# Kernel optimization log

Hardware: AMD Instinct MI355X
Metric: run time of the kernel (lower is better)

The kernel has to match this reference:

```python
import jax, jax.numpy as jnp
import numpy as np

H, D_MODEL, LEN_Q, LEN_K, D_K, D_V = 16, 1024, 512, 2048, 64, 64
B = 4

def setup_inputs() -> dict:
    key = jax.random.key(0)
    ks = jax.random.split(key, 16)
    s = 0.02
    return {
        "Q": jax.random.normal(ks[0], (B, LEN_Q, D_MODEL), jnp.float32),
        "K": jax.random.normal(ks[1], (B, LEN_K, D_MODEL), jnp.float32),
        "V": jax.random.normal(ks[2], (B, LEN_K, D_MODEL), jnp.float32),
        "node_num": LEN_Q,
        "mask": jax.random.randint(ks[3], (B, LEN_K), 0, 2, jnp.int32),
        # params (stored as [in, out] so y = x @ W + b)
        "Wq": jax.random.normal(ks[4], (D_MODEL, H * D_K), jnp.float32) * s,
        "bq": jnp.zeros((H * D_K,), jnp.float32),
        "Wk": jax.random.normal(ks[5], (D_MODEL, H * D_K), jnp.float32) * s,
        "bk": jnp.zeros((H * D_K,), jnp.float32),
        "Wv": jax.random.normal(ks[6], (D_MODEL, H * D_V), jnp.float32) * s,
        "bv": jnp.zeros((H * D_V,), jnp.float32),
        "Wo": jax.random.normal(ks[7], (H * D_V, D_MODEL), jnp.float32) * s,
        "bo": jnp.zeros((D_MODEL,), jnp.float32),
        "gamma": jnp.ones((D_MODEL,), jnp.float32),
        "beta": jnp.zeros((D_MODEL,), jnp.float32),
    }

def _layernorm(x, gamma, beta, eps=1e-5):
    mu = jnp.mean(x, axis=-1, keepdims=True)
    var = jnp.mean((x - mu) ** 2, axis=-1, keepdims=True)
    return (x - mu) * jax.lax.rsqrt(var + eps) * gamma + beta

def reference(Q, K, V, node_num, mask, Wq, bq, Wk, bk, Wv, bv, Wo, bo, gamma, beta):
    b, lq, _ = Q.shape
    lk = K.shape[1]
    q = (Q @ Wq + bq).reshape(b, lq, H, D_K)   # [B, Lq, h, dk]
    k = (K @ Wk + bk).reshape(b, lk, H, D_K)   # [B, Lk, h, dk]
    v = (V @ Wv + bv).reshape(b, lk, H, D_V)   # [B, Lk, h, dv]
    scores = jnp.einsum('bqhd,bkhd->bhqk', q, k) / jnp.sqrt(jnp.float32(D_K))
    scores = jnp.where(mask[:, None, None, :] == 0, -jnp.inf, scores)
    alpha = jax.nn.softmax(scores, axis=-1)    # [B, h, Lq, Lk]
    out = jnp.einsum('bhqk,bkhd->bqhd', alpha, v).reshape(b, lq, H * D_V)
    out = out @ Wo + bo + Q                    # dropout is identity (eval)
    return _layernorm(out, gamma, beta)
```

## Files before the change

### kernel.cpp

```cpp
#include <hip/hip_runtime.h>

typedef __attribute__((ext_vector_type(8))) __bf16 bf16x8;
typedef __attribute__((ext_vector_type(4))) float f32x4;
typedef __attribute__((ext_vector_type(8))) unsigned short u16x8;

__device__ __forceinline__ float bf2f(unsigned short h) {
  union { unsigned int u; float f; } a; a.u = ((unsigned int)h) << 16; return a.f;
}
__device__ __forceinline__ unsigned short f2bf(float f) {
  union { float f; unsigned int u; } a; a.f = f;
  unsigned int u = a.u;
  u += 0x7fffu + ((u >> 16) & 1u);
  return (unsigned short)(u >> 16);
}
__device__ __forceinline__ float fast_exp2(float x) {
#if __has_builtin(__builtin_amdgcn_exp2f)
  return __builtin_amdgcn_exp2f(x);
#else
  return exp2f(x);
#endif
}
__device__ __forceinline__ bf16x8 ld_frag(const unsigned short* p) {
  bf16x8 r; __builtin_memcpy(&r, p, 16); return r;
}
__device__ __forceinline__ void cp16(unsigned short* dst, const unsigned short* src) {
  u16x8 t; __builtin_memcpy(&t, src, 16); __builtin_memcpy(dst, &t, 16);
}

#if __has_builtin(__builtin_amdgcn_global_load_lds)
typedef __attribute__((address_space(3))) unsigned int lds_u32;
typedef const __attribute__((address_space(1))) unsigned int glb_u32;
__device__ __forceinline__ void gload16(const unsigned short* g, unsigned short* l) {
  __builtin_amdgcn_global_load_lds((glb_u32*)g, (lds_u32*)l, 16, 0, 0);
}
#else
__device__ __forceinline__ void gload16(const unsigned short* g, unsigned short* l) {
  cp16(l, g);
}
#endif

__global__ __launch_bounds__(256) void cvt_kernel(
    const float* __restrict__ in, unsigned short* __restrict__ out, int n8)
{
  int i = blockIdx.x * 256 + threadIdx.x;
  if (i >= n8) return;
  float tf[8]; __builtin_memcpy(tf, &in[(size_t)i * 8], 32);
  unsigned short tu[8];
#pragma unroll
  for (int j = 0; j < 8; j++) tu[j] = f2bf(tf[j]);
  __builtin_memcpy(&out[(size_t)i * 8], tu, 16);
}

__global__ __launch_bounds__(256) void transpose4_kernel(
    const float* __restrict__ w0, const float* __restrict__ w1,
    const float* __restrict__ w2, const float* __restrict__ w3,
    unsigned short* __restrict__ out)
{
  __shared__ unsigned short tile[64 * 65];
  const int z = blockIdx.z;
  const float* in = (z == 0) ? w0 : (z == 1) ? w1 : (z == 2) ? w2 : w3;
  unsigned short* o = out + (size_t)z * 1048576;
  const int dim = 1024;
  const int t = threadIdx.x;
  const int n0 = blockIdx.x * 64, k0 = blockIdx.y * 64;
#pragma unroll
  for (int e = 0; e < 16; e++) {
    int idx = e * 256 + t;
    int i = idx >> 6, j = idx & 63;
    tile[i * 65 + j] = f2bf(in[(size_t)(k0 + i) * dim + n0 + j]);
  }
  __syncthreads();
#pragma unroll
  for (int e = 0; e < 16; e++) {
    int idx = e * 256 + t;
    int i = idx >> 6, j = idx & 63;
    o[(size_t)(n0 + i) * dim + k0 + j] = tile[j * 65 + i];
  }
}

__global__ __launch_bounds__(256) void gemm_kt_kernel(
    const unsigned short* __restrict__ A,
    const unsigned short* __restrict__ BT,
    const float* __restrict__ bias,
    unsigned short* __restrict__ C,
    int M, int N, int K)
{
  __shared__ unsigned short As[2][128 * 32];
  __shared__ unsigned short Bs[2][128 * 32];
  const int tid  = threadIdx.x;
  const int wave = tid >> 6;
  const int lane = tid & 63;
  const int quad = lane >> 4;
  const int l16  = lane & 15;
  const int m0 = blockIdx.x * 128;
  const int n0 = blockIdx.y * 128;
  const int wm = (wave & 1) * 64;
  const int wn = (wave >> 1) * 64;

  const f32x4 fz = {0.0f, 0.0f, 0.0f, 0.0f};
  f32x4 acc[4][4];
#pragma unroll
  for (int i = 0; i < 4; i++)
#pragma unroll
    for (int j = 0; j < 4; j++) acc[i][j] = fz;

  const int srow0 = tid >> 2;
  const int srow1 = srow0 + 64;
  const int scol  = (tid & 3) * 8;

  auto stage = [&](int bf, int k0) {
    gload16(&A[(size_t)(m0 + srow0) * K + k0 + scol], &As[bf][srow0 * 32 + scol]);
    gload16(&A[(size_t)(m0 + srow1) * K + k0 + scol], &As[bf][srow1 * 32 + scol]);
    gload16(&BT[(size_t)(n0 + srow0) * K + k0 + scol], &Bs[bf][srow0 * 32 + scol]);
    gload16(&BT[(size_t)(n0 + srow1) * K + k0 + scol], &Bs[bf][srow1 * 32 + scol]);
  };

  const int NT = K >> 5;
  stage(0, 0);
  for (int kt = 0; kt < NT; ++kt) {
    const int cur = kt & 1;
    if (kt + 1 < NT) {
      stage(cur ^ 1, (kt + 1) << 5);
      asm volatile("s_waitcnt vmcnt(4)" ::: "memory");
    } else {
      asm volatile("s_waitcnt vmcnt(0)" ::: "memory");
    }
    __builtin_amdgcn_s_barrier();
    bf16x8 afr[4], bfr[4];
#pragma unroll
    for (int mt = 0; mt < 4; mt++) afr[mt] = ld_frag(&As[cur][(wm + mt * 16 + l16) * 32 + quad * 8]);
#pragma unroll
    for (int nt = 0; nt < 4; nt++) bfr[nt] = ld_frag(&Bs[cur][(wn + nt * 16 + l16) * 32 + quad * 8]);
#pragma unroll
    for (int mt = 0; mt < 4; mt++)
#pragma unroll
      for (int nt = 0; nt < 4; nt++)
        acc[mt][nt] = __builtin_amdgcn_mfma_f32_16x16x32_bf16(afr[mt], bfr[nt], acc[mt][nt], 0, 0, 0);
    __builtin_amdgcn_s_barrier();
  }

#pragma unroll
  for (int nt = 0; nt < 4; nt++) {
    const int col = n0 + wn + nt * 16 + l16;
    const float bvv = bias[col];
    const int h  = col >> 6;
    const int dk = col & 63;
    const int dkoff = (dk >> 5) * 512 + ((dk >> 3) & 3) * 8 + (dk & 7);
#pragma unroll
    for (int mt = 0; mt < 4; mt++) {
#pragma unroll
      for (int r = 0; r < 4; r++) {
        const int row = m0 + wm + mt * 16 + quad * 4 + r;
        const int bb = row >> 11, key = row & 2047;
        const size_t tile = ((size_t)((bb * 16 + h) * 32 + (key >> 6))) * 4096;
        C[tile + ((key & 63) >> 4) * 1024 + (key & 15) * 32 + dkoff] =
            f2bf(acc[mt][nt][r] + bvv);
      }
    }
  }
}

__global__ __launch_bounds__(256) void gemm_bt64_kernel(
    const unsigned short* __restrict__ A,
    const unsigned short* __restrict__ BT,
    const float* __restrict__ bias,
    unsigned short* __restrict__ C,
    int M, int N, int K, float cscale)
{
  __shared__ unsigned short As[2][64 * 32];
  __shared__ unsigned short Bs[2][128 * 32];
  const int tid  = threadIdx.x;
  const int wave = tid >> 6;
  const int lane = tid & 63;
  const int quad = lane >> 4;
  const int l16  = lane & 15;
  const int m0 = blockIdx.x * 64;
  const int n0 = blockIdx.y * 128;
  const int wm = (wave & 1) * 32;
  const int wn = (wave >> 1) * 64;

  const f32x4 fz = {0.0f, 0.0f, 0.0f, 0.0f};
  f32x4 acc[2][4];
#pragma unroll
  for (int i = 0; i < 2; i++)
#pragma unroll
    for (int j = 0; j < 4; j++) acc[i][j] = fz;

  const int srow0 = tid >> 2;
  const int srow1 = srow0 + 64;
  const int scol  = (tid & 3) * 8;

  auto stage = [&](int bf, int k0) {
    gload16(&A[(size_t)(m0 + srow0) * K + k0 + scol], &As[bf][srow0 * 32 + scol]);
    gload16(&BT[(size_t)(n0 + srow0) * K + k0 + scol], &Bs[bf][srow0 * 32 + scol]);
    gload16(&BT[(size_t)(n0 + srow1) * K + k0 + scol], &Bs[bf][srow1 * 32 + scol]);
  };

  const int NT = K >> 5;
  stage(0, 0);
  for (int kt = 0; kt < NT; ++kt) {
    const int cur = kt & 1;
    if (kt + 1 < NT) {
      stage(cur ^ 1, (kt + 1) << 5);
      asm volatile("s_waitcnt vmcnt(3)" ::: "memory");
    } else {
      asm volatile("s_waitcnt vmcnt(0)" ::: "memory");
    }
    __builtin_amdgcn_s_barrier();
    bf16x8 afr[2], bfr[4];
#pragma unroll
    for (int mt = 0; mt < 2; mt++) afr[mt] = ld_frag(&As[cur][(wm + mt * 16 + l16) * 32 + quad * 8]);
#pragma unroll
    for (int nt = 0; nt < 4; nt++) bfr[nt] = ld_frag(&Bs[cur][(wn + nt * 16 + l16) * 32 + quad * 8]);
#pragma unroll
    for (int mt = 0; mt < 2; mt++)
#pragma unroll
      for (int nt = 0; nt < 4; nt++)
        acc[mt][nt] = __builtin_amdgcn_mfma_f32_16x16x32_bf16(afr[mt], bfr[nt], acc[mt][nt], 0, 0, 0);
    __builtin_amdgcn_s_barrier();
  }

#pragma unroll
  for (int nt = 0; nt < 4; nt++) {
    int col = n0 + wn + nt * 16 + l16;
    float bv = bias[col];
#pragma unroll
    for (int mt = 0; mt < 2; mt++) {
      int rowb = m0 + wm + mt * 16 + quad * 4;
#pragma unroll
      for (int r = 0; r < 4; r++)
        C[(size_t)(rowb + r) * N + col] = f2bf((acc[mt][nt][r] + bv) * cscale);
    }
  }
}

__global__ __launch_bounds__(256) void gemm_vt_kernel(
    const unsigned short* __restrict__ A,
    const unsigned short* __restrict__ BT,
    const float* __restrict__ bias,
    unsigned short* __restrict__ vt)
{
  __shared__ unsigned short As[2][128 * 32];
  __shared__ unsigned short Bs[2][128 * 32];
  __shared__ unsigned short Ts[4][64 * 72];
  const int K = 1024;
  const int tid  = threadIdx.x;
  const int wave = tid >> 6;
  const int lane = tid & 63;
  const int quad = lane >> 4;
  const int l16  = lane & 15;
  const int m0 = blockIdx.x * 128;
  const int n0 = blockIdx.y * 128;
  const int wm = (wave & 1) * 64;
  const int wn = (wave >> 1) * 64;

  const f32x4 fz = {0.0f, 0.0f, 0.0f, 0.0f};
  f32x4 acc[4][4];
#pragma unroll
  for (int i = 0; i < 4; i++)
#pragma unroll
    for (int j = 0; j < 4; j++) acc[i][j] = fz;

  const int srow0 = tid >> 2;
  const int srow1 = srow0 + 64;
  const int scol  = (tid & 3) * 8;

  auto stage = [&](int bf, int k0) {
    gload16(&A[(size_t)(m0 + srow0) * K + k0 + scol], &As[bf][srow0 * 32 + scol]);
    gload16(&A[(size_t)(m0 + srow1) * K + k0 + scol], &As[bf][srow1 * 32 + scol]);
    gload16(&BT[(size_t)(n0 + srow0) * K + k0 + scol], &Bs[bf][srow0 * 32 + scol]);
    gload16(&BT[(size_t)(n0 + srow1) * K + k0 + scol], &Bs[bf][srow1 * 32 + scol]);
  };

  const int NT = K >> 5;
  stage(0, 0);
  for (int kt = 0; kt < NT; ++kt) {
    const int cur = kt & 1;
    if (kt + 1 < NT) {
      stage(cur ^ 1, (kt + 1) << 5);
      asm volatile("s_waitcnt vmcnt(4)" ::: "memory");
    } else {
      asm volatile("s_waitcnt vmcnt(0)" ::: "memory");
    }
    __builtin_amdgcn_s_barrier();
    bf16x8 afr[4], bfr[4];
#pragma unroll
    for (int mt = 0; mt < 4; mt++) afr[mt] = ld_frag(&As[cur][(wm + mt * 16 + l16) * 32 + quad * 8]);
#pragma unroll
    for (int nt = 0; nt < 4; nt++) bfr[nt] = ld_frag(&Bs[cur][(wn + nt * 16 + l16) * 32 + quad * 8]);
#pragma unroll
    for (int mt = 0; mt < 4; mt++)
#pragma unroll
      for (int nt = 0; nt < 4; nt++)
        acc[mt][nt] = __builtin_amdgcn_mfma_f32_16x16x32_bf16(afr[mt], bfr[nt], acc[mt][nt], 0, 0, 0);
    __builtin_amdgcn_s_barrier();
  }

#pragma unroll
  for (int nt = 0; nt < 4; nt++) {
    float bv = bias[n0 + wn + nt * 16 + l16];
#pragma unroll
    for (int mt = 0; mt < 4; mt++)
#pragma unroll
      for (int r = 0; r < 4; r++)
        Ts[wave][(nt * 16 + l16) * 72 + mt * 16 + quad * 4 + r] = f2bf(acc[mt][nt][r] + bv);
  }
  {
    const int R0 = m0 + wm;
    const int b  = R0 >> 11;
    const int key0 = R0 & 2047;
    const int h   = (n0 + wn) >> 6;
    const int dv  = lane;
    const int ktile = key0 >> 6;
    const size_t vtile = ((size_t)((b * 16 + h) * 32 + ktile)) * 4096;
    const size_t dbase = vtile + (size_t)(dv >> 4) * 1024 + (dv & 15) * 32;
#pragma unroll
    for (int jb = 0; jb < 8; jb++)
      cp16((unsigned short*)&vt[dbase + (jb >> 2) * 512 + (jb & 3) * 8],
           &Ts[wave][lane * 72 + jb * 8]);
  }
}

__global__ __launch_bounds__(256) void attn_kernel(
    const unsigned short* __restrict__ qp,
    const unsigned short* __restrict__ kp,
    const unsigned short* __restrict__ vt,
    const int* __restrict__ mask,
    unsigned short* __restrict__ attn)
{
  __shared__ unsigned short Kb[2][4096];
  __shared__ unsigned short Vb[2][4096];
  __shared__ int Ms[2048];
  __shared__ unsigned short Ps[4][16 * 72];

  const int tid  = threadIdx.x;
  const int wave = tid >> 6;
  const int lane = tid & 63;
  const int quad = lane >> 4;
  const int l16  = lane & 15;
  const int bid  = blockIdx.x;
  const int bh = bid & 63;
  const int qg = bid >> 6;
  const int b = bh >> 4, h = bh & 15;

  bf16x8 aq[2];
  {
    const size_t qbase = ((size_t)(b * 512 + qg * 64 + wave * 16 + l16)) * 1024 + h * 64;
#pragma unroll
    for (int kc = 0; kc < 2; kc++)
      aq[kc] = ld_frag(&qp[qbase + kc * 32 + quad * 8]);
  }
  {
    const unsigned short* mg = (const unsigned short*)(mask + b * 2048);
    unsigned short* ml = (unsigned short*)Ms;
    gload16(mg + tid * 8, ml + tid * 8);
    gload16(mg + 2048 + tid * 8, ml + 2048 + tid * 8);
  }
  asm volatile("s_waitcnt vmcnt(0)" ::: "memory");

  const size_t kvbase = (size_t)bh * 131072;
  auto stageKV = [&](int bf, int kt) {
    const unsigned short* ksrc = kp + kvbase + (size_t)kt * 4096;
    const unsigned short* vsrc = vt + kvbase + (size_t)kt * 4096;
    gload16(ksrc + tid * 8,        &Kb[bf][tid * 8]);
    gload16(ksrc + 2048 + tid * 8, &Kb[bf][2048 + tid * 8]);
    gload16(vsrc + tid * 8,        &Vb[bf][tid * 8]);
    gload16(vsrc + 2048 + tid * 8, &Vb[bf][2048 + tid * 8]);
  };

  const f32x4 fz = {0.0f, 0.0f, 0.0f, 0.0f};
  float l_i[4];
  f32x4 O[4];
#pragma unroll
  for (int r = 0; r < 4; r++) { l_i[r] = 0.0f; O[r] = fz; }

  stageKV(0, 0);
  for (int kt = 0; kt < 32; ++kt) {
    const int cur = kt & 1;
    if (kt + 1 < 32) {
      stageKV(cur ^ 1, kt + 1);
      asm volatile("s_waitcnt vmcnt(4)" ::: "memory");
    } else {
      asm volatile("s_waitcnt vmcnt(0)" ::: "memory");
    }
    __builtin_amdgcn_s_barrier();

    int mk[4];
#pragma unroll
    for (int nt = 0; nt < 4; nt++) mk[nt] = Ms[kt * 64 + nt * 16 + l16];

    f32x4 s[4];
#pragma unroll
    for (int nt = 0; nt < 4; nt++) s[nt] = fz;
    __builtin_amdgcn_s_setprio(1);
#pragma unroll
    for (int nt = 0; nt < 4; nt++)
#pragma unroll
      for (int kc = 0; kc < 2; kc++) {
        bf16x8 bk = ld_frag(&Kb[cur][nt * 1024 + kc * 512 + l16 * 32 + quad * 8]);
        s[nt] = __builtin_amdgcn_mfma_f32_16x16x32_bf16(aq[kc], bk, s[nt], 0, 0, 0);
      }
    __builtin_amdgcn_s_setprio(0);

#pragma unroll
    for (int nt = 0; nt < 4; nt++) {
      bool ok = (mk[nt] != 0);
#pragma unroll
      for (int r = 0; r < 4; r++) {
        float p = ok ? fast_exp2(s[nt][r]) : 0.0f;
        l_i[r] += p;
        Ps[wave][(quad * 4 + r) * 72 + nt * 16 + l16] = f2bf(p);
      }
    }

    bf16x8 ap[2];
#pragma unroll
    for (int kc = 0; kc < 2; kc++)
      ap[kc] = ld_frag(&Ps[wave][l16 * 72 + kc * 32 + quad * 8]);
    __builtin_amdgcn_s_setprio(1);
#pragma unroll
    for (int dvt = 0; dvt < 4; dvt++)
#pragma unroll
      for (int kc = 0; kc < 2; kc++) {
        bf16x8 bvf = ld_frag(&Vb[cur][dvt * 1024 + kc * 512 + l16 * 32 + quad * 8]);
        O[dvt] = __builtin_amdgcn_mfma_f32_16x16x32_bf16(ap[kc], bvf, O[dvt], 0, 0, 0);
      }
    __builtin_amdgcn_s_setprio(0);
    __builtin_amdgcn_s_barrier();
  }

#pragma unroll
  for (int off = 1; off < 16; off <<= 1)
#pragma unroll
    for (int r = 0; r < 4; r++) l_i[r] += __shfl_xor(l_i[r], off);

  const int growb = b * 512 + qg * 64 + wave * 16 + quad * 4;
#pragma unroll
  for (int r = 0; r < 4; r++) {
    const float inv = (l_i[r] > 0.0f) ? (1.0f / l_i[r]) : 0.0f;
#pragma unroll
    for (int dvt = 0; dvt < 4; dvt++)
      attn[(size_t)(growb + r) * 1024 + h * 64 + dvt * 16 + l16] = f2bf(O[dvt][r] * inv);
  }
}

__global__ __launch_bounds__(256) void ln_kernel(
    const unsigned short* __restrict__ x,
    const float* __restrict__ resid,
    const float* __restrict__ gamma,
    const float* __restrict__ beta,
    float* __restrict__ out)
{
  const int row = blockIdx.x;
  const int t = threadIdx.x;
  const int wave = t >> 6, lane = t & 63;
  __shared__ float red[8];
  float v[4];
  float s1 = 0.0f, s2 = 0.0f;
#pragma unroll
  for (int i = 0; i < 4; i++) {
    int e = t + i * 256;
    float val = bf2f(x[(size_t)row * 1024 + e]) + resid[(size_t)row * 1024 + e];
    v[i] = val; s1 += val; s2 += val * val;
  }
#pragma unroll
  for (int off = 1; off < 64; off <<= 1) { s1 += __shfl_xor(s1, off); s2 += __shfl_xor(s2, off); }
  if (lane == 0) { red[wave] = s1; red[4 + wave] = s2; }
  __syncthreads();
  s1 = red[0] + red[1] + red[2] + red[3];
  s2 = red[4] + red[5] + red[6] + red[7];
  float mu  = s1 * (1.0f / 1024.0f);
  float var = s2 * (1.0f / 1024.0f) - mu * mu;
  float rstd = rsqrtf(var + 1e-5f);
#pragma unroll
  for (int i = 0; i < 4; i++) {
    int e = t + i * 256;
    out[(size_t)row * 1024 + e] = (v[i] - mu) * rstd * gamma[e] + beta[e];
  }
}

extern "C" void kernel_launch(void* const* d_in, const int* in_sizes, int n_in,
                              void* d_out, int out_size, void* d_ws, size_t ws_size,
                              hipStream_t stream) {
  (void)out_size; (void)ws_size;
  const float* Q = (const float*)d_in[0];
  const float* K = (const float*)d_in[1];
  const float* V = (const float*)d_in[2];

  int ix = 3;
  if (ix < n_in && in_sizes[ix] == 1) ix++;
  const int* mask  = (const int*)d_in[ix++];
  const float* Wq = (const float*)d_in[ix++]; const float* bq = (const float*)d_in[ix++];
  const float* Wk = (const float*)d_in[ix++]; const float* bk = (const float*)d_in[ix++];
  const float* Wv = (const float*)d_in[ix++]; const float* bv = (const float*)d_in[ix++];
  const float* Wo = (const float*)d_in[ix++]; const float* bo = (const float*)d_in[ix++];
  const float* gm = (const float*)d_in[ix++]; const float* bt = (const float*)d_in[ix++];

  char* ws = (char*)d_ws;
  dim3 blk(256);

  unsigned short* WT4 = (unsigned short*)(ws);
  unsigned short* qp  = (unsigned short*)(ws + (8ull  << 20));
  unsigned short* kp  = (unsigned short*)(ws + (12ull << 20));
  unsigned short* vt  = (unsigned short*)(ws + (28ull << 20));
  unsigned short* at  = (unsigned short*)(ws + (44ull << 20));
  unsigned short* qb  = at;
  unsigned short* kvb = (unsigned short*)(ws + (48ull << 20));

  cvt_kernel<<<dim3(1024), blk, 0, stream>>>(Q, qb, 262144);
  cvt_kernel<<<dim3(4096), blk, 0, stream>>>(K, kvb, 1048576);
  transpose4_kernel<<<dim3(16, 16, 4), blk, 0, stream>>>(Wq, Wk, Wv, Wo, WT4);

  gemm_bt64_kernel<<<dim3(32, 8), blk, 0, stream>>>(qb, WT4, bq, qp, 2048, 1024, 1024, 0.18033688011112042f);
  gemm_kt_kernel<<<dim3(64, 8), blk, 0, stream>>>(kvb, WT4 + 1048576, bk, kp, 8192, 1024, 1024);
  cvt_kernel<<<dim3(4096), blk, 0, stream>>>(V, kvb, 1048576);
  gemm_vt_kernel<<<dim3(64, 8), blk, 0, stream>>>(kvb, WT4 + 2097152, bv, vt);

  attn_kernel<<<dim3(512), blk, 0, stream>>>(qp, kp, vt, mask, at);

  gemm_bt64_kernel<<<dim3(32, 8), blk, 0, stream>>>(at, WT4 + 3145728, bo, qp, 2048, 1024, 1024, 1.0f);
  ln_kernel<<<dim3(2048), blk, 0, stream>>>(qp, Q, gm, bt, (float*)d_out);
}
```

Before: 291.4 us.

## Relayout K/V tiles for contiguous fragment loads and use 512-thread attention blocks

Rewrites the K and V projection epilogues so each 16-byte MFMA fragment is laid out contiguously per lane, which lets the attention kernel read K/V fragments from LDS as lane*8. The attention kernel now runs 8 waves per block covering 128 queries, halving the grid and sharing each staged K/V tile across twice as many queries. Each thread issues one global-to-LDS load per tile instead of two. f2bf now uses the compiler's native bf16 conversion. The larger blocks lower the number of blocks per head and may reduce occupancy or load balance.

```diff
diff --git a/kernel.cpp b/kernel.cpp
--- a/kernel.cpp
+++ b/kernel.cpp
@@ -8,10 +8,8 @@
   union { unsigned int u; float f; } a; a.u = ((unsigned int)h) << 16; return a.f;
 }
 __device__ __forceinline__ unsigned short f2bf(float f) {
-  union { float f; unsigned int u; } a; a.f = f;
-  unsigned int u = a.u;
-  u += 0x7fffu + ((u >> 16) & 1u);
-  return (unsigned short)(u >> 16);
+  __bf16 h = (__bf16)f;
+  unsigned short u; __builtin_memcpy(&u, &h, 2); return u;
 }
 __device__ __forceinline__ float fast_exp2(float x) {
 #if __has_builtin(__builtin_amdgcn_exp2f)
@@ -145,7 +143,9 @@
     const float bvv = bias[col];
     const int h  = col >> 6;
     const int dk = col & 63;
-    const int dkoff = (dk >> 5) * 512 + ((dk >> 3) & 3) * 8 + (dk & 7);
+    const int kc = dk >> 5;
+    const int dq = (dk >> 3) & 3;
+    const int de = dk & 7;
 #pragma unroll
     for (int mt = 0; mt < 4; mt++) {
 #pragma unroll
@@ -153,7 +153,9 @@
         const int row = m0 + wm + mt * 16 + quad * 4 + r;
         const int bb = row >> 11, key = row & 2047;
         const size_t tile = ((size_t)((bb * 16 + h) * 32 + (key >> 6))) * 4096;
-        C[tile + ((key & 63) >> 4) * 1024 + (key & 15) * 32 + dkoff] =
+        const int knt = (key & 63) >> 4;
+        const int kl16 = key & 15;
+        C[tile + ((size_t)((knt * 2 + kc) * 64 + dq * 16 + kl16)) * 8 + de] =
             f2bf(acc[mt][nt][r] + bvv);
       }
     }
@@ -310,18 +312,18 @@
     const int b  = R0 >> 11;
     const int key0 = R0 & 2047;
     const int h   = (n0 + wn) >> 6;
-    const int dv  = lane;
     const int ktile = key0 >> 6;
     const size_t vtile = ((size_t)((b * 16 + h) * 32 + ktile)) * 4096;
-    const size_t dbase = vtile + (size_t)(dv >> 4) * 1024 + (dv & 15) * 32;
-#pragma unroll
-    for (int jb = 0; jb < 8; jb++)
-      cp16((unsigned short*)&vt[dbase + (jb >> 2) * 512 + (jb & 3) * 8],
-           &Ts[wave][lane * 72 + jb * 8]);
-  }
-}
-
-__global__ __launch_bounds__(256) void attn_kernel(
+#pragma unroll
+    for (int jb = 0; jb < 8; jb++) {
+      const size_t dst = vtile +
+          ((size_t)(((lane >> 4) * 2 + (jb >> 2)) * 64 + (jb & 3) * 16 + (lane & 15))) * 8;
+      cp16((unsigned short*)&vt[dst], &Ts[wave][lane * 72 + jb * 8]);
+    }
+  }
+}
+
+__global__ __launch_bounds__(512) void attn_kernel(
     const unsigned short* __restrict__ qp,
     const unsigned short* __restrict__ kp,
     const unsigned short* __restrict__ vt,
@@ -331,7 +333,7 @@
   __shared__ unsigned short Kb[2][4096];
   __shared__ unsigned short Vb[2][4096];
   __shared__ int Ms[2048];
-  __shared__ unsigned short Ps[4][16 * 72];
+  __shared__ unsigned short Ps[8][16 * 72];
 
   const int tid  = threadIdx.x;
   const int wave = tid >> 6;
@@ -345,7 +347,7 @@
 
   bf16x8 aq[2];
   {
-    const size_t qbase = ((size_t)(b * 512 + qg * 64 + wave * 16 + l16)) * 1024 + h * 64;
+    const size_t qbase = ((size_t)(b * 512 + qg * 128 + wave * 16 + l16)) * 1024 + h * 64;
 #pragma unroll
     for (int kc = 0; kc < 2; kc++)
       aq[kc] = ld_frag(&qp[qbase + kc * 32 + quad * 8]);
@@ -354,7 +356,6 @@
     const unsigned short* mg = (const unsigned short*)(mask + b * 2048);
     unsigned short* ml = (unsigned short*)Ms;
     gload16(mg + tid * 8, ml + tid * 8);
-    gload16(mg + 2048 + tid * 8, ml + 2048 + tid * 8);
   }
   asm volatile("s_waitcnt vmcnt(0)" ::: "memory");
 
@@ -362,10 +363,8 @@
   auto stageKV = [&](int bf, int kt) {
     const unsigned short* ksrc = kp + kvbase + (size_t)kt * 4096;
     const unsigned short* vsrc = vt + kvbase + (size_t)kt * 4096;
-    gload16(ksrc + tid * 8,        &Kb[bf][tid * 8]);
-    gload16(ksrc + 2048 + tid * 8, &Kb[bf][2048 + tid * 8]);
-    gload16(vsrc + tid * 8,        &Vb[bf][tid * 8]);
-    gload16(vsrc + 2048 + tid * 8, &Vb[bf][2048 + tid * 8]);
+    gload16(ksrc + tid * 8, &Kb[bf][tid * 8]);
+    gload16(vsrc + tid * 8, &Vb[bf][tid * 8]);
   };
 
   const f32x4 fz = {0.0f, 0.0f, 0.0f, 0.0f};
@@ -379,7 +378,7 @@
     const int cur = kt & 1;
     if (kt + 1 < 32) {
       stageKV(cur ^ 1, kt + 1);
-      asm volatile("s_waitcnt vmcnt(4)" ::: "memory");
+      asm volatile("s_waitcnt vmcnt(2)" ::: "memory");
     } else {
       asm volatile("s_waitcnt vmcnt(0)" ::: "memory");
     }
@@ -397,7 +396,7 @@
     for (int nt = 0; nt < 4; nt++)
 #pragma unroll
       for (int kc = 0; kc < 2; kc++) {
-        bf16x8 bk = ld_frag(&Kb[cur][nt * 1024 + kc * 512 + l16 * 32 + quad * 8]);
+        bf16x8 bk = ld_frag(&Kb[cur][(nt * 2 + kc) * 512 + lane * 8]);
         s[nt] = __builtin_amdgcn_mfma_f32_16x16x32_bf16(aq[kc], bk, s[nt], 0, 0, 0);
       }
     __builtin_amdgcn_s_setprio(0);
@@ -422,7 +421,7 @@
     for (int dvt = 0; dvt < 4; dvt++)
 #pragma unroll
       for (int kc = 0; kc < 2; kc++) {
-        bf16x8 bvf = ld_frag(&Vb[cur][dvt * 1024 + kc * 512 + l16 * 32 + quad * 8]);
+        bf16x8 bvf = ld_frag(&Vb[cur][(dvt * 2 + kc) * 512 + lane * 8]);
         O[dvt] = __builtin_amdgcn_mfma_f32_16x16x32_bf16(ap[kc], bvf, O[dvt], 0, 0, 0);
       }
     __builtin_amdgcn_s_setprio(0);
@@ -434,7 +433,7 @@
 #pragma unroll
     for (int r = 0; r < 4; r++) l_i[r] += __shfl_xor(l_i[r], off);
 
-  const int growb = b * 512 + qg * 64 + wave * 16 + quad * 4;
+  const int growb = b * 512 + qg * 128 + wave * 16 + quad * 4;
 #pragma unroll
   for (int r = 0; r < 4; r++) {
     const float inv = (l_i[r] > 0.0f) ? (1.0f / l_i[r]) : 0.0f;
@@ -498,6 +497,7 @@
 
   char* ws = (char*)d_ws;
   dim3 blk(256);
+  dim3 blk512(512);
 
   unsigned short* WT4 = (unsigned short*)(ws);
   unsigned short* qp  = (unsigned short*)(ws + (8ull  << 20));
@@ -516,7 +516,7 @@
   cvt_kernel<<<dim3(4096), blk, 0, stream>>>(V, kvb, 1048576);
   gemm_vt_kernel<<<dim3(64, 8), blk, 0, stream>>>(kvb, WT4 + 2097152, bv, vt);
 
-  attn_kernel<<<dim3(512), blk, 0, stream>>>(qp, kp, vt, mask, at);
+  attn_kernel<<<dim3(256), blk512, 0, stream>>>(qp, kp, vt, mask, at);
 
   gemm_bt64_kernel<<<dim3(32, 8), blk, 0, stream>>>(at, WT4 + 3145728, bo, qp, 2048, 1024, 1024, 1.0f);
   ln_kernel<<<dim3(2048), blk, 0, stream>>>(qp, Q, gm, bt, (float*)d_out);
```

New measurement: 287.0 us. About the same (-1.5%).
